# Performance work log

Measured on AMD Instinct MI355X. Metric: run time of the kernel, lower is better.

The kernel has to match this reference:

```python
import jax, jax.numpy as jnp
import numpy as np
from jax import lax

N, D, H = 8192, 256, 128
EPS = 1e-5


def _layernorm(x, g, b):
    m = jnp.mean(x, axis=-1, keepdims=True)
    v = jnp.mean((x - m) ** 2, axis=-1, keepdims=True)
    return (x - m) * jax.lax.rsqrt(v + EPS) * g + b


def setup_inputs() -> dict:
    key = jax.random.key(0)
    ks = jax.random.split(key, 8)
    s = 1.0 / np.sqrt(D)
    return {
        "x": jax.random.normal(ks[0], (N, D), jnp.float32),
        "wq": jax.random.normal(ks[1], (D, D), jnp.float32) * s,
        "bq": jnp.zeros((D,), jnp.float32),
        "wk": jax.random.normal(ks[2], (D, D), jnp.float32) * s,
        "bk": jnp.zeros((D,), jnp.float32),
        "wv": jax.random.normal(ks[3], (D, D), jnp.float32) * s,
        "bv": jnp.zeros((D,), jnp.float32),
        "cw": jax.random.normal(ks[4], (1, 1, 3, 3), jnp.float32) / 3.0,
        "cb": jnp.zeros((1,), jnp.float32),
        "m1w": jax.random.normal(ks[5], (H, D), jnp.float32) * s,
        "m2w": jax.random.normal(ks[6], (D, H), jnp.float32) / np.sqrt(H),
        "bng": jnp.ones((H,), jnp.float32),
        "bnb": jnp.zeros((H,), jnp.float32),
        "ln1g": jnp.ones((D,), jnp.float32),
        "ln1b": jnp.zeros((D,), jnp.float32),
        "ln2g": jnp.ones((D,), jnp.float32),
        "ln2b": jnp.zeros((D,), jnp.float32),
    }


def reference(x, wq, bq, wk, bk, wv, bv, cw, cb, m1w, m2w, bng, bnb, ln1g, ln1b, ln2g, ln2b):
    q = x @ wq.T + bq            # [N, D]
    k = x @ wk.T + bk
    v = x @ wv.T + bv
    # global Frobenius-norm normalization (torch.norm(q, p=2) over whole tensor)
    q = q / jnp.linalg.norm(q)
    k = k / jnp.linalg.norm(k)
    A = q @ k.T                  # [N, N]
    # 3x3 conv2d, 1->1 channel, padding SAME
    A4 = A[None, None, :, :]
    A4 = lax.conv_general_dilated(A4, cw, window_strides=(1, 1), padding="SAME")
    A4 = A4 + cb[None, :, None, None]
    agg_A = A4[0, 0]             # [N, N]
    attn = agg_A @ v             # [N, D]
    h = x + _layernorm(attn, ln1g, ln1b)
    # MLP with BatchNorm1d (training-mode batch stats, biased var)
    z = _layernorm(h, ln2g, ln2b) @ m1w.T          # [N, H]
    mu = jnp.mean(z, axis=0)
    var = jnp.mean((z - mu) ** 2, axis=0)
    z = (z - mu) * jax.lax.rsqrt(var + EPS) * bng + bnb
    z = jax.nn.relu(z)
    out = h + z @ m2w.T
    return out
```

## Files before the change

kernel.cpp:

```cpp
#include <hip/hip_runtime.h>
#include <hip/hip_bf16.h>
#include <math.h>


#define N_ 8192
#define D_ 256
#define H_ 128
#define EPSF 1e-5f

typedef unsigned short ushort_t;
typedef unsigned int uint_t;
typedef __attribute__((ext_vector_type(8))) short bf16x8;
typedef __attribute__((ext_vector_type(4))) short bf16x4;
typedef __attribute__((ext_vector_type(4))) float f32x4;

static const size_t OFF_QB  = 0;
static const size_t OFF_KT  = 4195328;
static const size_t OFF_VT  = 8389632;
static const size_t OFF_GP  = 12588032;
static const size_t OFF_MT  = 25170944;
static const size_t OFF_SVP = 25564160;
static const size_t OFF_SVC = 25826304;
static const size_t OFF_RED = 25827328;
static const size_t OFF_ZSP = 25829376;
static const size_t OFF_BNS = 26353664;
static const size_t WS_NEED = 26354688;

#define VT_S 8200

__device__ __forceinline__ ushort_t f2bf(float f) {
    __hip_bfloat16 h = __float2bfloat16(f);
    return reinterpret_cast<ushort_t&>(h);
}

__device__ __forceinline__ bf16x8 cvt8(float4 f0, float4 f1) {
    bf16x8 o;
    o[0] = (short)f2bf(f0.x); o[1] = (short)f2bf(f0.y);
    o[2] = (short)f2bf(f0.z); o[3] = (short)f2bf(f0.w);
    o[4] = (short)f2bf(f1.x); o[5] = (short)f2bf(f1.y);
    o[6] = (short)f2bf(f1.z); o[7] = (short)f2bf(f1.w);
    return o;
}

__device__ __forceinline__ float waveSum(float v)
{
#pragma unroll
    for (int o = 32; o > 0; o >>= 1) v += __shfl_xor(v, o);
    return v;
}

__global__ void __launch_bounds__(256)
qkv_mfma(const float* __restrict__ x,
         const float* __restrict__ wq, const float* __restrict__ bq,
         const float* __restrict__ wk, const float* __restrict__ bk,
         const float* __restrict__ wv, const float* __restrict__ bv,
         ushort_t* __restrict__ QbG, ushort_t* __restrict__ KT,
         ushort_t* __restrict__ VT,
         float* __restrict__ RED, float* __restrict__ SVP)
{
    __shared__ ushort_t XS[32][264];
    __shared__ ushort_t WS[256][40];
    __shared__ float lds4[4];
    const int tid = threadIdx.x, lane = tid & 63, wid = tid >> 6;
    const int sel = blockIdx.y;
    const int i0 = blockIdx.x * 32;
    const int jw = wid * 64;
    const int l15 = lane & 15, kg = lane >> 4;
    const float* W = (sel == 0) ? wq : ((sel == 1) ? wk : wv);
    const float* B = (sel == 0) ? bq : ((sel == 1) ? bk : bv);

    if (sel == 0 && blockIdx.x == 0) {
        QbG[tid] = 0; QbG[(size_t)8193 * 256 + tid] = 0;
        VT[(size_t)tid * VT_S] = 0; VT[(size_t)tid * VT_S + 8193] = 0;
    }

#pragma unroll
    for (int p = 0; p < 4; ++p) {
        int lin = p * 256 + tid;
        int row = lin >> 5;
        int c8  = (lin & 31) * 8;
        const float* xp = x + (size_t)(i0 + row) * 256 + c8;
        *(bf16x8*)(&XS[row][c8]) = cvt8(*(const float4*)xp, *(const float4*)(xp + 4));
    }

    f32x4 acc[2][4];
#pragma unroll
    for (int mi = 0; mi < 2; ++mi)
#pragma unroll
        for (int ni = 0; ni < 4; ++ni) acc[mi][ni] = 0.0f;

    for (int k0 = 0; k0 < 256; k0 += 32) {
        __syncthreads();
#pragma unroll
        for (int p = 0; p < 4; ++p) {
            int j  = p * 64 + (tid >> 2);
            int c8 = (tid & 3) * 8;
            const float* wp = W + (size_t)j * 256 + k0 + c8;
            *(bf16x8*)(&WS[j][c8]) = cvt8(*(const float4*)wp, *(const float4*)(wp + 4));
        }
        __syncthreads();

        bf16x8 a[2], b[4];
#pragma unroll
        for (int mi = 0; mi < 2; ++mi)
            a[mi] = *(const bf16x8*)(&XS[16 * mi + l15][k0 + 8 * kg]);
#pragma unroll
        for (int ni = 0; ni < 4; ++ni)
            b[ni] = *(const bf16x8*)(&WS[jw + 16 * ni + l15][8 * kg]);
#pragma unroll
        for (int mi = 0; mi < 2; ++mi)
#pragma unroll
            for (int ni = 0; ni < 4; ++ni)
                acc[mi][ni] = __builtin_amdgcn_mfma_f32_16x16x32_bf16(a[mi], b[ni], acc[mi][ni], 0, 0, 0);
    }

    float ssq = 0.0f;
    float colp[4] = {0.0f, 0.0f, 0.0f, 0.0f};

    if (sel == 0) {
#pragma unroll
        for (int mi = 0; mi < 2; ++mi)
#pragma unroll
            for (int ni = 0; ni < 4; ++ni) {
                const int col = jw + 16 * ni + l15;
                const float bias = B[col];
#pragma unroll
                for (int r = 0; r < 4; ++r) {
                    const int row = i0 + 16 * mi + 4 * kg + r;
                    float val = acc[mi][ni][r] + bias;
                    QbG[(size_t)(row + 1) * 256 + col] = f2bf(val);
                    ssq = fmaf(val, val, ssq);
                }
            }
    } else if (sel == 1) {
#pragma unroll
        for (int mi = 0; mi < 2; ++mi)
#pragma unroll
            for (int ni = 0; ni < 4; ++ni) {
                const int col = jw + 16 * ni + l15;
                const float bias = B[col];
                const int tb = i0 + 16 * mi + 4 * kg;
                bf16x4 pk;
#pragma unroll
                for (int r = 0; r < 4; ++r) {
                    float val = acc[mi][ni][r] + bias;
                    ssq = fmaf(val, val, ssq);
                    pk[r] = (short)f2bf(val);
                }
                *(bf16x4*)(KT + (size_t)col * 8192 + tb) = pk;
            }
    } else {
#pragma unroll
        for (int mi = 0; mi < 2; ++mi)
#pragma unroll
            for (int ni = 0; ni < 4; ++ni) {
                const int col = jw + 16 * ni + l15;
                const float bias = B[col];
                const int tb = i0 + 16 * mi + 4 * kg;
                float v0 = acc[mi][ni][0] + bias, v1 = acc[mi][ni][1] + bias;
                float v2 = acc[mi][ni][2] + bias, v3 = acc[mi][ni][3] + bias;
                colp[ni] += v0 + v1 + v2 + v3;
                ushort_t* p = VT + (size_t)col * VT_S + tb + 1;
                p[0] = f2bf(v0);
                *(uint_t*)(p + 1) = (uint_t)f2bf(v1) | ((uint_t)f2bf(v2) << 16);
                p[3] = f2bf(v3);
            }
    }

    if (sel < 2) {
        float s = ssq;
#pragma unroll
        for (int o = 32; o > 0; o >>= 1) s += __shfl_down(s, o);
        if (lane == 0) lds4[wid] = s;
        __syncthreads();
        if (tid == 0)
            RED[sel * 256 + blockIdx.x] = lds4[0] + lds4[1] + lds4[2] + lds4[3];
    } else {
#pragma unroll
        for (int ni = 0; ni < 4; ++ni) {
            float v = colp[ni];
            v += __shfl_xor(v, 16);
            v += __shfl_xor(v, 32);
            if (kg == 0)
                SVP[(size_t)blockIdx.x * 256 + jw + 16 * ni + l15] = v;
        }
    }
}

__global__ void __launch_bounds__(256)
g_mfma(const ushort_t* __restrict__ KT, const ushort_t* __restrict__ VT,
       float* __restrict__ GP)
{
    const int tid = threadIdx.x, lane = tid & 63, wid = tid >> 6;
    const int d0 = blockIdx.x * 64 + (wid >> 1) * 32;
    const int jw = blockIdx.y * 32 + (wid & 1) * 16;
    const int ks = blockIdx.z;
    const int l15 = lane & 15, kg = lane >> 4;

    f32x4 acc[3][2];
#pragma unroll
    for (int v = 0; v < 3; ++v) { acc[v][0] = 0.0f; acc[v][1] = 0.0f; }

    for (int tt = 0; tt < 512; tt += 32) {
        const int t0 = ks * 512 + tt;
        bf16x8 a[2];
#pragma unroll
        for (int mi = 0; mi < 2; ++mi)
            a[mi] = *(const bf16x8*)(KT + (size_t)(d0 + 16 * mi + l15) * 8192 + t0 + 8 * kg);

        const ushort_t* vp = VT + (size_t)(jw + l15) * VT_S + t0 + 8 * kg;
        uint4 r0 = *(const uint4*)vp;
        uint4 r2 = *(const uint4*)(vp + 2);
        uint4 m1;
        m1.x = (r0.x >> 16) | (r2.x << 16);
        m1.y = (r0.y >> 16) | (r2.y << 16);
        m1.z = (r0.z >> 16) | (r2.z << 16);
        m1.w = (r0.w >> 16) | (r2.w << 16);
        bf16x8 b2 = __builtin_bit_cast(bf16x8, r0);
        bf16x8 b0 = __builtin_bit_cast(bf16x8, r2);
        bf16x8 b1 = __builtin_bit_cast(bf16x8, m1);
#pragma unroll
        for (int mi = 0; mi < 2; ++mi) {
            acc[0][mi] = __builtin_amdgcn_mfma_f32_16x16x32_bf16(a[mi], b0, acc[0][mi], 0, 0, 0);
            acc[1][mi] = __builtin_amdgcn_mfma_f32_16x16x32_bf16(a[mi], b1, acc[1][mi], 0, 0, 0);
            acc[2][mi] = __builtin_amdgcn_mfma_f32_16x16x32_bf16(a[mi], b2, acc[2][mi], 0, 0, 0);
        }
    }

#pragma unroll
    for (int v = 0; v < 3; ++v) {
        float* gp = GP + (size_t)(ks * 3 + v) * 65536;
#pragma unroll
        for (int mi = 0; mi < 2; ++mi)
#pragma unroll
            for (int r = 0; r < 4; ++r)
                gp[(size_t)(d0 + 16 * mi + 4 * kg + r) * 256 + (jw + l15)]
                    = acc[v][mi][r];
    }
}

__global__ void combine_m(const float* __restrict__ GP, const float* __restrict__ cw,
                          const float* __restrict__ RED, const float* __restrict__ SVP,
                          const float* __restrict__ cb,
                          ushort_t* __restrict__ MTc, float* __restrict__ SVC)
{
    __shared__ float lds8[8];
    __shared__ float scsh;
    const int d = blockIdx.x, j = threadIdx.x;

    float sq = RED[j], sk = RED[256 + j];
#pragma unroll
    for (int o = 32; o > 0; o >>= 1) { sq += __shfl_down(sq, o); sk += __shfl_down(sk, o); }
    if ((j & 63) == 0) { lds8[j >> 6] = sq; lds8[4 + (j >> 6)] = sk; }

    float g[3] = {0.0f, 0.0f, 0.0f};
    for (int ks = 0; ks < 16; ++ks)
#pragma unroll
        for (int v = 0; v < 3; ++v)
            g[v] += GP[(size_t)(ks * 3 + v) * 65536 + (size_t)d * 256 + j];

    __syncthreads();
    if (j == 0) {
        float SQ = lds8[0] + lds8[1] + lds8[2] + lds8[3];
        float SK = lds8[4] + lds8[5] + lds8[6] + lds8[7];
        scsh = rsqrtf(SQ) * rsqrtf(SK);
    }
    __syncthreads();
    const float sc = scsh;

#pragma unroll
    for (int u = 0; u < 3; ++u) {
        float m = sc * (cw[u * 3 + 0] * g[0] + cw[u * 3 + 1] * g[1] + cw[u * 3 + 2] * g[2]);
        MTc[(size_t)u * 65536 + (size_t)(d >> 3) * 2048 + (size_t)j * 8 + (d & 7)]
            = f2bf(m);
    }
    if (d == 0) {
        float s = 0.0f;
        for (int b = 0; b < 256; ++b) s += SVP[(size_t)b * 256 + j];
        SVC[j] = cb[0] * s;
    }
}

__global__ void __launch_bounds__(512)
attn_ln_z_mfma(const ushort_t* __restrict__ QbG, const ushort_t* __restrict__ MTc,
               const float* __restrict__ SVC, const float* __restrict__ x,
               const float* __restrict__ ln1g, const float* __restrict__ ln1b,
               const float* __restrict__ ln2g, const float* __restrict__ ln2b,
               const float* __restrict__ m1w,
               float* __restrict__ h, float* __restrict__ Z,
               float* __restrict__ ZSP)
{
    __shared__ ushort_t QS[18][264];
    __shared__ float OUT[16][260];
    __shared__ ushort_t WS[128][40];
    const int tid = threadIdx.x, lane = tid & 63, wid = tid >> 6;
    const int i0 = blockIdx.x * 16;
    const int jw = wid * 32;
    const int l15 = lane & 15, kg = lane >> 4;

    float4 xpre0 = *(const float4*)(x + (size_t)(i0 + wid * 2 + 0) * 256 + lane * 4);
    float4 xpre1 = *(const float4*)(x + (size_t)(i0 + wid * 2 + 1) * 256 + lane * 4);

    {
        int row = tid >> 5, c8 = (tid & 31) * 8;
        *(bf16x8*)(&QS[row][c8]) = *(const bf16x8*)(QbG + (size_t)(i0 + row) * 256 + c8);
        int idx = tid + 512;
        if (idx < 576) {
            row = idx >> 5; c8 = (idx & 31) * 8;
            *(bf16x8*)(&QS[row][c8]) = *(const bf16x8*)(QbG + (size_t)(i0 + row) * 256 + c8);
        }
    }
    __syncthreads();

    f32x4 acc[2];
    acc[0] = 0.0f; acc[1] = 0.0f;

    for (int k0 = 0; k0 < 256; k0 += 32) {
        bf16x8 a[3], b[3][2];
#pragma unroll
        for (int u = 0; u < 3; ++u)
            a[u] = *(const bf16x8*)(&QS[l15 + u][k0 + 8 * kg]);
#pragma unroll
        for (int u = 0; u < 3; ++u)
#pragma unroll
            for (int ni = 0; ni < 2; ++ni)
                b[u][ni] = *(const bf16x8*)(MTc + (size_t)u * 65536
                    + (size_t)((k0 >> 3) + kg) * 2048
                    + (size_t)(jw + 16 * ni + l15) * 8);
#pragma unroll
        for (int ni = 0; ni < 2; ++ni)
#pragma unroll
            for (int u = 0; u < 3; ++u)
                acc[ni] = __builtin_amdgcn_mfma_f32_16x16x32_bf16(
                    a[u], b[u][ni], acc[ni], 0, 0, 0);
    }

#pragma unroll
    for (int ni = 0; ni < 2; ++ni) {
        const int col = jw + 16 * ni + l15;
        const float sv = SVC[col];
#pragma unroll
        for (int r = 0; r < 4; ++r)
            OUT[4 * kg + r][col] = acc[ni][r] + sv;
    }
    __syncthreads();

    const float4 g14 = *(const float4*)(ln1g + lane * 4);
    const float4 b14 = *(const float4*)(ln1b + lane * 4);
    const float4 g24 = *(const float4*)(ln2g + lane * 4);
    const float4 b24 = *(const float4*)(ln2b + lane * 4);
#pragma unroll
    for (int rr = 0; rr < 2; ++rr) {
        const int row_l = wid * 2 + rr;
        const size_t off = (size_t)(i0 + row_l) * 256 + lane * 4;

        float4 a4 = *(const float4*)&OUT[row_l][lane * 4];
        float m = waveSum(a4.x + a4.y + a4.z + a4.w) * (1.0f / D_);
        float4 d4 = make_float4(a4.x - m, a4.y - m, a4.z - m, a4.w - m);
        float var = waveSum(d4.x * d4.x + d4.y * d4.y + d4.z * d4.z + d4.w * d4.w) * (1.0f / D_);
        float rs = rsqrtf(var + EPSF);

        float4 x4 = (rr == 0) ? xpre0 : xpre1;
        float4 h4;
        h4.x = x4.x + d4.x * rs * g14.x + b14.x;
        h4.y = x4.y + d4.y * rs * g14.y + b14.y;
        h4.z = x4.z + d4.z * rs * g14.z + b14.z;
        h4.w = x4.w + d4.w * rs * g14.w + b14.w;
        *(float4*)(h + off) = h4;

        float m2 = waveSum(h4.x + h4.y + h4.z + h4.w) * (1.0f / D_);
        float4 e4 = make_float4(h4.x - m2, h4.y - m2, h4.z - m2, h4.w - m2);
        float v2 = waveSum(e4.x * e4.x + e4.y * e4.y + e4.z * e4.z + e4.w * e4.w) * (1.0f / D_);
        float rs2 = rsqrtf(v2 + EPSF);

        float4 o4;
        o4.x = e4.x * rs2 * g24.x + b24.x;
        o4.y = e4.y * rs2 * g24.y + b24.y;
        o4.z = e4.z * rs2 * g24.z + b24.z;
        o4.w = e4.w * rs2 * g24.w + b24.w;
        *(float4*)&OUT[row_l][lane * 4] = o4;
    }
    __syncthreads();

    const int jz = wid * 16;
    f32x4 zacc;
    zacc = 0.0f;

    for (int k0 = 0; k0 < 256; k0 += 32) {
        if (k0) __syncthreads();
        {
            int j  = tid >> 2;
            int c8 = (tid & 3) * 8;
            const float* wp = m1w + (size_t)j * 256 + k0 + c8;
            *(bf16x8*)(&WS[j][c8]) = cvt8(*(const float4*)wp, *(const float4*)(wp + 4));
        }
        __syncthreads();

        bf16x8 a, b;
        {
            const float* lp = &OUT[l15][k0 + 8 * kg];
            a = cvt8(*(const float4*)lp, *(const float4*)(lp + 4));
        }
        b = *(const bf16x8*)(&WS[jz + l15][8 * kg]);
        zacc = __builtin_amdgcn_mfma_f32_16x16x32_bf16(a, b, zacc, 0, 0, 0);
    }

    float s = 0.0f, q = 0.0f;
    const int col = jz + l15;
#pragma unroll
    for (int r = 0; r < 4; ++r) {
        float zv = zacc[r];
        Z[(size_t)(i0 + 4 * kg + r) * 128 + col] = zv;
        s += zv;
        q = fmaf(zv, zv, q);
    }
    s += __shfl_xor(s, 16); s += __shfl_xor(s, 32);
    q += __shfl_xor(q, 16); q += __shfl_xor(q, 32);
    if (kg == 0) {
        ZSP[(size_t)blockIdx.x * 256 + col] = s;
        ZSP[(size_t)blockIdx.x * 256 + 128 + col] = q;
    }
}

__global__ void bn_reduce(const float* __restrict__ ZSP, float* __restrict__ BNS)
{
    __shared__ float red[8][32];
    const int tid = threadIdx.x;
    const int c0 = blockIdx.x * 32;
    const int cl = tid & 31, g = tid >> 5;
    float s = 0.0f;
    for (int b = g; b < 512; b += 8)
        s += ZSP[(size_t)b * 256 + c0 + cl];
    red[g][cl] = s;
    __syncthreads();
    if (tid < 32) {
        float t = 0.0f;
#pragma unroll
        for (int g2 = 0; g2 < 8; ++g2) t += red[g2][tid];
        BNS[c0 + tid] = t;
    }
}

__global__ void __launch_bounds__(512)
gemm_out_mfma(const float* __restrict__ Z, const float* __restrict__ W,
              const float* __restrict__ BNS,
              const float* __restrict__ bng, const float* __restrict__ bnb,
              float* __restrict__ out)
{
    __shared__ float bnA[128], bnB[128];
    __shared__ ushort_t XS[16][136];
    __shared__ ushort_t WS2[256][40];
    const int tid = threadIdx.x, lane = tid & 63, wid = tid >> 6;
    const int i0 = blockIdx.x * 16;
    const int jw = wid * 32;
    const int l15 = lane & 15, kg = lane >> 4;

    float oprev[2][4];
#pragma unroll
    for (int ni = 0; ni < 2; ++ni)
#pragma unroll
        for (int r = 0; r < 4; ++r)
            oprev[ni][r] = out[(size_t)(i0 + 4 * kg + r) * 256 + jw + 16 * ni + l15];

    if (tid < 128) {
        float s = BNS[tid], q = BNS[128 + tid];
        float mu = s * (1.0f / N_);
        float var = q * (1.0f / N_) - mu * mu;
        float aa = rsqrtf(var + EPSF) * bng[tid];
        bnA[tid] = aa;
        bnB[tid] = bnb[tid] - mu * aa;
    }
    __syncthreads();

    if (tid < 256) {
        int row = tid >> 4, c8 = (tid & 15) * 8;
        const float* zp = Z + (size_t)(i0 + row) * 128 + c8;
        float4 f0 = *(const float4*)zp;
        float4 f1 = *(const float4*)(zp + 4);
        float4 g0, g1;
        g0.x = fmaxf(fmaf(f0.x, bnA[c8 + 0], bnB[c8 + 0]), 0.0f);
        g0.y = fmaxf(fmaf(f0.y, bnA[c8 + 1], bnB[c8 + 1]), 0.0f);
        g0.z = fmaxf(fmaf(f0.z, bnA[c8 + 2], bnB[c8 + 2]), 0.0f);
        g0.w = fmaxf(fmaf(f0.w, bnA[c8 + 3], bnB[c8 + 3]), 0.0f);
        g1.x = fmaxf(fmaf(f1.x, bnA[c8 + 4], bnB[c8 + 4]), 0.0f);
        g1.y = fmaxf(fmaf(f1.y, bnA[c8 + 5], bnB[c8 + 5]), 0.0f);
        g1.z = fmaxf(fmaf(f1.z, bnA[c8 + 6], bnB[c8 + 6]), 0.0f);
        g1.w = fmaxf(fmaf(f1.w, bnA[c8 + 7], bnB[c8 + 7]), 0.0f);
        *(bf16x8*)(&XS[row][c8]) = cvt8(g0, g1);
    }

    f32x4 acc[2];
    acc[0] = 0.0f; acc[1] = 0.0f;

    for (int k0 = 0; k0 < 128; k0 += 32) {
        __syncthreads();
#pragma unroll
        for (int p = 0; p < 2; ++p) {
            int idx = p * 512 + tid;
            int j  = idx >> 2;
            int c8 = (idx & 3) * 8;
            const float* wp = W + (size_t)j * 128 + k0 + c8;
            *(bf16x8*)(&WS2[j][c8]) = cvt8(*(const float4*)wp, *(const float4*)(wp + 4));
        }
        __syncthreads();

        bf16x8 a = *(const bf16x8*)(&XS[l15][k0 + 8 * kg]);
        bf16x8 b[2];
#pragma unroll
        for (int ni = 0; ni < 2; ++ni)
            b[ni] = *(const bf16x8*)(&WS2[jw + 16 * ni + l15][8 * kg]);
#pragma unroll
        for (int ni = 0; ni < 2; ++ni)
            acc[ni] = __builtin_amdgcn_mfma_f32_16x16x32_bf16(a, b[ni], acc[ni], 0, 0, 0);
    }

#pragma unroll
    for (int ni = 0; ni < 2; ++ni)
#pragma unroll
        for (int r = 0; r < 4; ++r) {
            const size_t idx = (size_t)(i0 + 4 * kg + r) * 256
                             + (jw + 16 * ni + l15);
            out[idx] = oprev[ni][r] + acc[ni][r];
        }
}

extern "C" void kernel_launch(void* const* d_in, const int* in_sizes, int n_in,
                              void* d_out, int out_size, void* d_ws, size_t ws_size,
                              hipStream_t stream)
{
    const float* x    = (const float*)d_in[0];
    const float* wq   = (const float*)d_in[1];
    const float* bq   = (const float*)d_in[2];
    const float* wk   = (const float*)d_in[3];
    const float* bk   = (const float*)d_in[4];
    const float* wv   = (const float*)d_in[5];
    const float* bv   = (const float*)d_in[6];
    const float* cw   = (const float*)d_in[7];
    const float* cb   = (const float*)d_in[8];
    const float* m1w  = (const float*)d_in[9];
    const float* m2w  = (const float*)d_in[10];
    const float* bng  = (const float*)d_in[11];
    const float* bnb  = (const float*)d_in[12];
    const float* ln1g = (const float*)d_in[13];
    const float* ln1b = (const float*)d_in[14];
    const float* ln2g = (const float*)d_in[15];
    const float* ln2b = (const float*)d_in[16];

    float* outF = (float*)d_out;
    char*  wsb  = (char*)d_ws;
    if (ws_size < WS_NEED) return;

    ushort_t* QbG = (ushort_t*)(wsb + OFF_QB);
    ushort_t* KT  = (ushort_t*)(wsb + OFF_KT);
    ushort_t* VT  = (ushort_t*)(wsb + OFF_VT);
    float*    GP  = (float*)(wsb + OFF_GP);
    ushort_t* MTc = (ushort_t*)(wsb + OFF_MT);
    float*    SVP = (float*)(wsb + OFF_SVP);
    float*    SVC = (float*)(wsb + OFF_SVC);
    float*    RED = (float*)(wsb + OFF_RED);
    float*    ZSP = (float*)(wsb + OFF_ZSP);
    float*    BNS = (float*)(wsb + OFF_BNS);
    float*    Z   = (float*)(wsb + OFF_GP);

    const dim3 b256(256);
    const dim3 b512(512);

    qkv_mfma<<<dim3(256, 3), b256, 0, stream>>>(x, wq, bq, wk, bk, wv, bv,
                                                QbG, KT, VT, RED, SVP);
    g_mfma<<<dim3(4, 8, 16), b256, 0, stream>>>(KT, VT, GP);
    combine_m<<<256, b256, 0, stream>>>(GP, cw, RED, SVP, cb, MTc, SVC);
    attn_ln_z_mfma<<<512, b512, 0, stream>>>(QbG, MTc, SVC, x,
                                             ln1g, ln1b, ln2g, ln2b, m1w,
                                             outF, Z, ZSP);
    bn_reduce<<<8, b256, 0, stream>>>(ZSP, BNS);
    gemm_out_mfma<<<512, b512, 0, stream>>>(Z, m2w, BNS, bng, bnb, outF);
}
```

Baseline: 94.34 us.

## Pre-convert weights to bf16 MFMA-fragment layout and load directly from global

Adds a prep kernel that converts wq/wk/wv, m1w and m2w to bf16 once per call, in a k-block-major layout that matches the MFMA B-fragment. The three GEMM kernels then read B operands straight from global/L2 and no longer stage fp32 weights through LDS with per-k-step barriers and conversions. This removes repeated conversion work and most __syncthreads in the inner loops. The cost is an extra kernel launch and global-memory latency on B loads in place of LDS reads.

```diff
diff --git a/kernel.cpp b/kernel.cpp
--- a/kernel.cpp
+++ b/kernel.cpp
@@ -24,7 +24,10 @@
 static const size_t OFF_RED = 25827328;
 static const size_t OFF_ZSP = 25829376;
 static const size_t OFF_BNS = 26353664;
-static const size_t WS_NEED = 26354688;
+static const size_t OFF_WC  = 26354688;
+static const size_t OFF_M1C = 26747904;
+static const size_t OFF_M2C = 26813440;
+static const size_t WS_NEED = 26878976;
 
 #define VT_S 8200
 
@@ -49,30 +52,55 @@
     return v;
 }
 
+__global__ void prep_w(const float* __restrict__ wq, const float* __restrict__ wk,
+                       const float* __restrict__ wv, const float* __restrict__ m1w,
+                       const float* __restrict__ m2w,
+                       ushort_t* __restrict__ WC, ushort_t* __restrict__ M1C,
+                       ushort_t* __restrict__ M2C,
+                       ushort_t* __restrict__ QbG, ushort_t* __restrict__ VT)
+{
+    const int bid = blockIdx.x, tid = threadIdx.x;
+    if (bid < 96) {
+        const int sel = bid >> 5, kb = bid & 31;
+        const float* W = (sel == 0) ? wq : ((sel == 1) ? wk : wv);
+        const float* p = W + (size_t)tid * 256 + kb * 8;
+        *(bf16x8*)(WC + (size_t)sel * 65536 + (size_t)kb * 2048 + (size_t)tid * 8)
+            = cvt8(*(const float4*)p, *(const float4*)(p + 4));
+    } else if (bid < 128) {
+        const int kb = bid - 96;
+        if (tid < 128) {
+            const float* p = m1w + (size_t)tid * 256 + kb * 8;
+            *(bf16x8*)(M1C + (size_t)kb * 1024 + (size_t)tid * 8)
+                = cvt8(*(const float4*)p, *(const float4*)(p + 4));
+        }
+    } else if (bid < 144) {
+        const int kb = bid - 128;
+        const float* p = m2w + (size_t)tid * 128 + kb * 8;
+        *(bf16x8*)(M2C + (size_t)kb * 2048 + (size_t)tid * 8)
+            = cvt8(*(const float4*)p, *(const float4*)(p + 4));
+    } else {
+        QbG[tid] = 0; QbG[(size_t)8193 * 256 + tid] = 0;
+        VT[(size_t)tid * VT_S] = 0; VT[(size_t)tid * VT_S + 8193] = 0;
+    }
+}
+
 __global__ void __launch_bounds__(256)
-qkv_mfma(const float* __restrict__ x,
-         const float* __restrict__ wq, const float* __restrict__ bq,
-         const float* __restrict__ wk, const float* __restrict__ bk,
-         const float* __restrict__ wv, const float* __restrict__ bv,
+qkv_mfma(const float* __restrict__ x, const ushort_t* __restrict__ WC,
+         const float* __restrict__ bq, const float* __restrict__ bk,
+         const float* __restrict__ bv,
          ushort_t* __restrict__ QbG, ushort_t* __restrict__ KT,
          ushort_t* __restrict__ VT,
          float* __restrict__ RED, float* __restrict__ SVP)
 {
     __shared__ ushort_t XS[32][264];
-    __shared__ ushort_t WS[256][40];
     __shared__ float lds4[4];
     const int tid = threadIdx.x, lane = tid & 63, wid = tid >> 6;
     const int sel = blockIdx.y;
     const int i0 = blockIdx.x * 32;
     const int jw = wid * 64;
     const int l15 = lane & 15, kg = lane >> 4;
-    const float* W = (sel == 0) ? wq : ((sel == 1) ? wk : wv);
+    const ushort_t* Wc = WC + (size_t)sel * 65536;
     const float* B = (sel == 0) ? bq : ((sel == 1) ? bk : bv);
-
-    if (sel == 0 && blockIdx.x == 0) {
-        QbG[tid] = 0; QbG[(size_t)8193 * 256 + tid] = 0;
-        VT[(size_t)tid * VT_S] = 0; VT[(size_t)tid * VT_S + 8193] = 0;
-    }
 
 #pragma unroll
     for (int p = 0; p < 4; ++p) {
@@ -82,6 +110,7 @@
         const float* xp = x + (size_t)(i0 + row) * 256 + c8;
         *(bf16x8*)(&XS[row][c8]) = cvt8(*(const float4*)xp, *(const float4*)(xp + 4));
     }
+    __syncthreads();
 
     f32x4 acc[2][4];
 #pragma unroll
@@ -90,23 +119,14 @@
         for (int ni = 0; ni < 4; ++ni) acc[mi][ni] = 0.0f;
 
     for (int k0 = 0; k0 < 256; k0 += 32) {
-        __syncthreads();
-#pragma unroll
-        for (int p = 0; p < 4; ++p) {
-            int j  = p * 64 + (tid >> 2);
-            int c8 = (tid & 3) * 8;
-            const float* wp = W + (size_t)j * 256 + k0 + c8;
-            *(bf16x8*)(&WS[j][c8]) = cvt8(*(const float4*)wp, *(const float4*)(wp + 4));
-        }
-        __syncthreads();
-
         bf16x8 a[2], b[4];
 #pragma unroll
         for (int mi = 0; mi < 2; ++mi)
             a[mi] = *(const bf16x8*)(&XS[16 * mi + l15][k0 + 8 * kg]);
 #pragma unroll
         for (int ni = 0; ni < 4; ++ni)
-            b[ni] = *(const bf16x8*)(&WS[jw + 16 * ni + l15][8 * kg]);
+            b[ni] = *(const bf16x8*)(Wc + (size_t)((k0 >> 3) + kg) * 2048
+                                        + (size_t)(jw + 16 * ni + l15) * 8);
 #pragma unroll
         for (int mi = 0; mi < 2; ++mi)
 #pragma unroll
@@ -286,13 +306,12 @@
                const float* __restrict__ SVC, const float* __restrict__ x,
                const float* __restrict__ ln1g, const float* __restrict__ ln1b,
                const float* __restrict__ ln2g, const float* __restrict__ ln2b,
-               const float* __restrict__ m1w,
+               const ushort_t* __restrict__ M1C,
                float* __restrict__ h, float* __restrict__ Z,
                float* __restrict__ ZSP)
 {
     __shared__ ushort_t QS[18][264];
     __shared__ float OUT[16][260];
-    __shared__ ushort_t WS[128][40];
     const int tid = threadIdx.x, lane = tid & 63, wid = tid >> 6;
     const int i0 = blockIdx.x * 16;
     const int jw = wid * 32;
@@ -387,21 +406,13 @@
     zacc = 0.0f;
 
     for (int k0 = 0; k0 < 256; k0 += 32) {
-        if (k0) __syncthreads();
-        {
-            int j  = tid >> 2;
-            int c8 = (tid & 3) * 8;
-            const float* wp = m1w + (size_t)j * 256 + k0 + c8;
-            *(bf16x8*)(&WS[j][c8]) = cvt8(*(const float4*)wp, *(const float4*)(wp + 4));
-        }
-        __syncthreads();
-
         bf16x8 a, b;
         {
             const float* lp = &OUT[l15][k0 + 8 * kg];
             a = cvt8(*(const float4*)lp, *(const float4*)(lp + 4));
         }
-        b = *(const bf16x8*)(&WS[jz + l15][8 * kg]);
+        b = *(const bf16x8*)(M1C + (size_t)((k0 >> 3) + kg) * 1024
+                                  + (size_t)(jz + l15) * 8);
         zacc = __builtin_amdgcn_mfma_f32_16x16x32_bf16(a, b, zacc, 0, 0, 0);
     }
 
@@ -442,14 +453,13 @@
 }
 
 __global__ void __launch_bounds__(512)
-gemm_out_mfma(const float* __restrict__ Z, const float* __restrict__ W,
+gemm_out_mfma(const float* __restrict__ Z, const ushort_t* __restrict__ M2C,
               const float* __restrict__ BNS,
               const float* __restrict__ bng, const float* __restrict__ bnb,
               float* __restrict__ out)
 {
     __shared__ float bnA[128], bnB[128];
     __shared__ ushort_t XS[16][136];
-    __shared__ ushort_t WS2[256][40];
     const int tid = threadIdx.x, lane = tid & 63, wid = tid >> 6;
     const int i0 = blockIdx.x * 16;
     const int jw = wid * 32;
@@ -488,27 +498,18 @@
         g1.w = fmaxf(fmaf(f1.w, bnA[c8 + 7], bnB[c8 + 7]), 0.0f);
         *(bf16x8*)(&XS[row][c8]) = cvt8(g0, g1);
     }
+    __syncthreads();
 
     f32x4 acc[2];
     acc[0] = 0.0f; acc[1] = 0.0f;
 
     for (int k0 = 0; k0 < 128; k0 += 32) {
-        __syncthreads();
-#pragma unroll
-        for (int p = 0; p < 2; ++p) {
-            int idx = p * 512 + tid;
-            int j  = idx >> 2;
-            int c8 = (idx & 3) * 8;
-            const float* wp = W + (size_t)j * 128 + k0 + c8;
-            *(bf16x8*)(&WS2[j][c8]) = cvt8(*(const float4*)wp, *(const float4*)(wp + 4));
-        }
-        __syncthreads();
-
         bf16x8 a = *(const bf16x8*)(&XS[l15][k0 + 8 * kg]);
         bf16x8 b[2];
 #pragma unroll
         for (int ni = 0; ni < 2; ++ni)
-            b[ni] = *(const bf16x8*)(&WS2[jw + 16 * ni + l15][8 * kg]);
+            b[ni] = *(const bf16x8*)(M2C + (size_t)((k0 >> 3) + kg) * 2048
+                                          + (size_t)(jw + 16 * ni + l15) * 8);
 #pragma unroll
         for (int ni = 0; ni < 2; ++ni)
             acc[ni] = __builtin_amdgcn_mfma_f32_16x16x32_bf16(a, b[ni], acc[ni], 0, 0, 0);
@@ -560,18 +561,22 @@
     float*    RED = (float*)(wsb + OFF_RED);
     float*    ZSP = (float*)(wsb + OFF_ZSP);
     float*    BNS = (float*)(wsb + OFF_BNS);
+    ushort_t* WC  = (ushort_t*)(wsb + OFF_WC);
+    ushort_t* M1C = (ushort_t*)(wsb + OFF_M1C);
+    ushort_t* M2C = (ushort_t*)(wsb + OFF_M2C);
     float*    Z   = (float*)(wsb + OFF_GP);
 
     const dim3 b256(256);
     const dim3 b512(512);
 
-    qkv_mfma<<<dim3(256, 3), b256, 0, stream>>>(x, wq, bq, wk, bk, wv, bv,
+    prep_w<<<145, b256, 0, stream>>>(wq, wk, wv, m1w, m2w, WC, M1C, M2C, QbG, VT);
+    qkv_mfma<<<dim3(256, 3), b256, 0, stream>>>(x, WC, bq, bk, bv,
                                                 QbG, KT, VT, RED, SVP);
     g_mfma<<<dim3(4, 8, 16), b256, 0, stream>>>(KT, VT, GP);
     combine_m<<<256, b256, 0, stream>>>(GP, cw, RED, SVP, cb, MTc, SVC);
     attn_ln_z_mfma<<<512, b512, 0, stream>>>(QbG, MTc, SVC, x,
-                                             ln1g, ln1b, ln2g, ln2b, m1w,
+                                             ln1g, ln1b, ln2g, ln2b, M1C,
                                              outF, Z, ZSP);
     bn_reduce<<<8, b256, 0, stream>>>(ZSP, BNS);
-    gemm_out_mfma<<<512, b512, 0, stream>>>(Z, m2w, BNS, bng, bnb, outF);
-}
+    gemm_out_mfma<<<512, b512, 0, stream>>>(Z, M2C, BNS, bng, bnb, outF);
+}
```

After: 88.57 us. 6.1% less time.
